# Kernel tuning notes

Measured on AMD Instinct MI355X. Metric: run time of the kernel, lower is better.

The kernel has to match this reference:

```python
import jax, jax.numpy as jnp
import numpy as np

TOP_K = 2
NUM_EXPERTS = 64
SEQ, BS, HS = 2048, 4, 4096
TOKENS = SEQ * BS  # tokens_per_batch
TOL = 1e-4
EPS = 1e-8


def sinkhorn(temp_cost):
    # temp_cost: (T, E) float32 logits. Mirrors SinkhornRouter.sinkhorn exactly.
    cost = jnp.exp(temp_cost)
    n0, n1 = cost.shape
    # initial d0 (overwritten inside loop in torch too, kept for fidelity of carry dtype/shape)
    d0 = (TOKENS / NUM_EXPERTS) * jnp.sum(jnp.exp(2.0 * temp_cost), axis=1)
    d1 = jnp.ones((n1,), dtype=cost.dtype)
    err0 = jnp.asarray(1e9, dtype=cost.dtype)

    def cond(carry):
        _, _, err = carry
        return err > TOL

    def body(carry):
        d0, d1, _ = carry  # d1 here plays the role of d1_old
        d0_new = (1.0 / n0) / (jnp.sum(d1 * cost, axis=1) + EPS)          # (T,)
        d1_new = (1.0 / n1) / (jnp.sum(d0_new[:, None] * cost, axis=0) + EPS)  # (E,)
        err = jnp.mean(jnp.abs(d1 - d1_new))
        return (d0_new, d1_new, err)

    d0, d1, _ = jax.lax.while_loop(cond, body, (d0, d1, err0))
    return d1 * cost * d0[:, None]


def setup_inputs() -> dict:
    key = jax.random.key(0)
    kx, kw = jax.random.split(key)
    x = jax.random.normal(kx, (SEQ, BS, HS), dtype=jnp.float32)
    W = jax.random.normal(kw, (NUM_EXPERTS, HS), dtype=jnp.float32) * 0.02
    return {"x": x, "W": W}


def reference(x, W):
    # router logits: (T, E)
    logits = jnp.reshape(x, (-1, x.shape[-1])) @ W.T
    # Sinkhorn normalization is done in fp32 under no_grad in torch -> stop_gradient
    norm_logits = sinkhorn(jax.lax.stop_gradient(logits).astype(jnp.float32))
    _, indices = jax.lax.top_k(norm_logits, TOP_K)  # (T, top_k) int32
    # top_k > 1 -> softmax activation (fp32, cast back)
    probs = jax.nn.softmax(logits.astype(jnp.float32), axis=-1).astype(logits.dtype)
    scores = jnp.take_along_axis(probs, indices, axis=1)  # (T, top_k)
    return scores, indices
```

## Files before the change

### kernel.cpp

```cpp
#include <hip/hip_runtime.h>
#include <hip/hip_cooperative_groups.h>
#include <math.h>

namespace cg = cooperative_groups;

namespace {
constexpr int kTokens = 8192;
constexpr int kHS = 4096;
constexpr float kTol = 1e-4f;
constexpr float kEps = 1e-8f;
constexpr int kMaxIters = 1000;
constexpr int kSinkBlocks = 32;
constexpr int kSplit = 4;
constexpr size_t kTagFloats = 128;
constexpr size_t kGdataFloats = 2 * 32 * 64;
constexpr size_t kPartOff = kTagFloats + kGdataFloats;
constexpr size_t kPartFloats = (size_t)kTokens * kSplit * 64;
constexpr size_t kWhiOff = kPartOff + kPartFloats;
constexpr size_t kWFragFloats = (size_t)(kHS / 32) * 4 * 64 * 4;
constexpr size_t kWloOff = kWhiOff + kWFragFloats;
constexpr size_t kWsNeedFloats = kWloOff + kWFragFloats;
constexpr size_t kWtpFloats = (size_t)(kHS / 4) * 64 * 4;
}

__device__ __forceinline__ float wave_sum(float v) {
#pragma unroll
  for (int o = 32; o; o >>= 1) v += __shfl_xor(v, o, 64);
  return v;
}

typedef __attribute__((ext_vector_type(8))) short bf16x8;
typedef __attribute__((ext_vector_type(4))) float f32x4;

__device__ __forceinline__ unsigned short f2bf(float x) {
  unsigned u = __builtin_bit_cast(unsigned, x);
  u += 0x7fffu + ((u >> 16) & 1u);
  return (unsigned short)(u >> 16);
}

__device__ __forceinline__ void split8r(const float4 a, const float4 b,
                                        bf16x8& hi, bf16x8& lo) {
  const float v[8] = {a.x, a.y, a.z, a.w, b.x, b.y, b.z, b.w};
#pragma unroll
  for (int j = 0; j < 8; ++j) {
    const unsigned short h = f2bf(v[j]);
    const float hf = __builtin_bit_cast(float, (unsigned)h << 16);
    hi[j] = (short)h;
    lo[j] = (short)f2bf(v[j] - hf);
  }
}

__device__ __forceinline__ void split8(const float* p, bf16x8& hi, bf16x8& lo) {
  split8r(*(const float4*)p, *(const float4*)(p + 4), hi, lo);
}

__global__ void __launch_bounds__(256)
k_wsplit(const float* __restrict__ W, bf16x8* __restrict__ whi,
         bf16x8* __restrict__ wlo) {
  const int idx = blockIdx.x * 256 + threadIdx.x;
  const int lane = idx & 63;
  const int n = (idx >> 6) & 3;
  const int kk = idx >> 8;
  const int e = 16 * n + (lane & 15);
  const int k = kk * 32 + ((lane >> 4) << 3);
  bf16x8 hi, lo;
  split8(W + (size_t)e * kHS + k, hi, lo);
  whi[idx] = hi;
  wlo[idx] = lo;
}

__device__ __forceinline__ void ldB(const bf16x8* __restrict__ bhp,
                                    const bf16x8* __restrict__ blp, int ks,
                                    bf16x8 (&bh)[4], bf16x8 (&bl)[4]) {
#pragma unroll
  for (int n = 0; n < 4; ++n) {
    bh[n] = bhp[(ks * 4 + n) * 64];
    bl[n] = blp[(ks * 4 + n) * 64];
  }
}

__device__ __forceinline__ void ldX(const float* __restrict__ xp, int ks,
                                    float4 (&x)[2][2]) {
#pragma unroll
  for (int m = 0; m < 2; ++m) {
    x[m][0] = *(const float4*)(xp + (size_t)(16 * m) * kHS + ks * 32);
    x[m][1] = *(const float4*)(xp + (size_t)(16 * m) * kHS + ks * 32 + 4);
  }
}

__device__ __forceinline__ void mstep(const float4 (&x)[2][2],
                                      const bf16x8 (&bh)[4],
                                      const bf16x8 (&bl)[4],
                                      f32x4 (&acc)[2][4]) {
#pragma unroll
  for (int m = 0; m < 2; ++m) {
    bf16x8 ah, al;
    split8r(x[m][0], x[m][1], ah, al);
#pragma unroll
    for (int n = 0; n < 4; ++n) {
      acc[m][n] =
          __builtin_amdgcn_mfma_f32_16x16x32_bf16(ah, bh[n], acc[m][n], 0, 0, 0);
      acc[m][n] =
          __builtin_amdgcn_mfma_f32_16x16x32_bf16(al, bh[n], acc[m][n], 0, 0, 0);
      acc[m][n] =
          __builtin_amdgcn_mfma_f32_16x16x32_bf16(ah, bl[n], acc[m][n], 0, 0, 0);
    }
  }
}

__global__ void __launch_bounds__(256, 3)
k_logits(const float* __restrict__ X, const bf16x8* __restrict__ whi,
         const bf16x8* __restrict__ wlo, float* __restrict__ part) {
  const int tid = threadIdx.x;
  const int lane = tid & 63;
  const int wid = tid >> 6;
  const int tile = blockIdx.x >> 2;
  const int sig = blockIdx.x & 3;
  const int t0 = tile * 32;
  const int r = lane & 15;
  const int g = lane >> 4;
  const int kk0 = sig * 32 + wid * 8;

  const float* xp = X + (size_t)(t0 + r) * kHS + kk0 * 32 + g * 8;
  const bf16x8* bhp = whi + (size_t)kk0 * 4 * 64 + lane;
  const bf16x8* blp = wlo + (size_t)kk0 * 4 * 64 + lane;

  f32x4 acc[2][4];
#pragma unroll
  for (int m = 0; m < 2; ++m)
#pragma unroll
    for (int n = 0; n < 4; ++n) acc[m][n] = (f32x4){0.f, 0.f, 0.f, 0.f};

  bf16x8 bhA[4], blA[4], bhB[4], blB[4];
  float4 xA[2][2], xB[2][2];
  ldB(bhp, blp, 0, bhA, blA);
  ldX(xp, 0, xA);

#pragma unroll
  for (int kp = 0; kp < 4; ++kp) {
    const int ks = 2 * kp;
    ldB(bhp, blp, ks + 1, bhB, blB);
    ldX(xp, ks + 1, xB);
    mstep(xA, bhA, blA, acc);
    if (ks + 2 < 8) {
      ldB(bhp, blp, ks + 2, bhA, blA);
      ldX(xp, ks + 2, xA);
    }
    mstep(xB, bhB, blB, acc);
  }

  __shared__ __align__(16) float red[4][32][68];
#pragma unroll
  for (int m = 0; m < 2; ++m)
#pragma unroll
    for (int n = 0; n < 4; ++n)
#pragma unroll
      for (int q = 0; q < 4; ++q)
        red[wid][m * 16 + g * 4 + q][n * 16 + r] = acc[m][n][q];
  __syncthreads();

#pragma unroll
  for (int rep = 0; rep < 2; ++rep) {
    const int idx = rep * 256 + tid;
    const int t = idx >> 4;
    const int e4 = (idx & 15) * 4;
    float4 s = *(const float4*)&red[0][t][e4];
#pragma unroll
    for (int w = 1; w < 4; ++w) {
      const float4 p = *(const float4*)&red[w][t][e4];
      s.x += p.x; s.y += p.y; s.z += p.z; s.w += p.w;
    }
    *(float4*)(part + ((size_t)(tile * 4 + sig) * 32 + t) * 64 + e4) = s;
  }
}

__global__ void __launch_bounds__(1024, 1)
k_sinkhorn(const float* __restrict__ part, float* __restrict__ out,
           unsigned* __restrict__ tags, float* __restrict__ gdata) {
  const int tid = threadIdx.x;
  const int lane = tid & 63;
  const int wid = __builtin_amdgcn_readfirstlane(tid >> 6);
  const int blk = blockIdx.x;
  __shared__ float lds[1024];

  const int t0 = blk * 256 + wid * 16;
  float lg[16], cst[16];
#pragma unroll
  for (int t = 0; t < 16; ++t) {
    const int row = t0 + t;
    const float* pb =
        part + ((size_t)(row >> 5) * (kSplit * 32) + (row & 31)) * 64 + lane;
    const float a = pb[0] + pb[2048] + pb[4096] + pb[6144];
    lg[t] = a;
    cst[t] = expf(a);
  }

  float d1 = 1.0f;
  float d0v[16];
  for (int it = 0; it < kMaxIters; ++it) {
    float p = 0.0f;
#pragma unroll
    for (int t = 0; t < 16; ++t) {
      const float s = wave_sum(d1 * cst[t]);
      const float d0t = (1.0f / 8192.0f) / (s + kEps);
      d0v[t] = d0t;
      p = fmaf(d0t, cst[t], p);
    }
    __syncthreads();
    lds[wid * 64 + lane] = p;
    __syncthreads();
    const unsigned want = (unsigned)(it + 1);
    const int buf = it & 1;
    if (wid == 0) {
      float bp = 0.0f;
#pragma unroll
      for (int w = 0; w < 16; ++w) bp += lds[w * 64 + lane];
      __hip_atomic_store(&gdata[((size_t)buf * 32 + blk) * 64 + lane], bp,
                         __ATOMIC_RELAXED, __HIP_MEMORY_SCOPE_AGENT);
      __threadfence();
      if (lane == 0)
        __hip_atomic_store(&tags[buf * 32 + blk], want, __ATOMIC_RELEASE,
                           __HIP_MEMORY_SCOPE_AGENT);
      if (lane < 32) {
        while (__hip_atomic_load(&tags[buf * 32 + lane], __ATOMIC_ACQUIRE,
                                 __HIP_MEMORY_SCOPE_AGENT) != want) {
          __builtin_amdgcn_s_sleep(1);
        }
      }
    }
    __syncthreads();
    float s2 = 0.0f;
#pragma unroll
    for (int i = 0; i < 2; ++i)
      s2 += __hip_atomic_load(
          &gdata[((size_t)buf * 32 + wid * 2 + i) * 64 + lane],
          __ATOMIC_RELAXED, __HIP_MEMORY_SCOPE_AGENT);
    lds[wid * 64 + lane] = s2;
    __syncthreads();
    float colsum = 0.0f;
#pragma unroll
    for (int w = 0; w < 16; ++w) colsum += lds[w * 64 + lane];
    const float d1n = (1.0f / 64.0f) / (colsum + kEps);
    const float err = wave_sum(fabsf(d1 - d1n)) * (1.0f / 64.0f);
    d1 = d1n;
    if (err <= kTol) break;
  }

#pragma unroll
  for (int t = 0; t < 16; ++t) {
    const float lgv = lg[t];
    float m = lgv;
#pragma unroll
    for (int o = 32; o; o >>= 1) m = fmaxf(m, __shfl_xor(m, o, 64));
    const float ex = expf(lgv - m);
    const float den = wave_sum(ex);
    const float prob = ex / den;

    const float v = (d1 * cst[t]) * d0v[t];
    float v1 = v;
    int i1 = lane;
#pragma unroll
    for (int o = 32; o; o >>= 1) {
      const float ov = __shfl_xor(v1, o, 64);
      const int oi = __shfl_xor(i1, o, 64);
      if (ov > v1 || (ov == v1 && oi < i1)) { v1 = ov; i1 = oi; }
    }
    float v2 = (lane == i1) ? -INFINITY : v;
    int i2 = lane;
#pragma unroll
    for (int o = 32; o; o >>= 1) {
      const float ov = __shfl_xor(v2, o, 64);
      const int oi = __shfl_xor(i2, o, 64);
      if (ov > v2 || (ov == v2 && oi < i2)) { v2 = ov; i2 = oi; }
    }
    const float p1 = __shfl(prob, i1, 64);
    const float p2 = __shfl(prob, i2, 64);
    if (lane == 0) {
      const int row = t0 + t;
      out[row * 2 + 0] = p1;
      out[row * 2 + 1] = p2;
      out[2 * kTokens + row * 2 + 0] = (float)i1;
      out[2 * kTokens + row * 2 + 1] = (float)i2;
    }
  }
}

__global__ void __launch_bounds__(256, 1)
sinkhorn_router(const float* __restrict__ X, const float* __restrict__ W,
                float* __restrict__ out, float* __restrict__ ws) {
  cg::grid_group grid = cg::this_grid();
  const int tid = threadIdx.x;
  const int lane = tid & 63;
  const int wid = __builtin_amdgcn_readfirstlane(tid >> 6);
  const int blk = blockIdx.x;

  float4* wtp = reinterpret_cast<float4*>(ws);
  float* gpart = ws + kWtpFloats;
  __shared__ float lds[256];

  {
    const int j = blk * 256 + tid;
    const int e = j & 63;
    const int k4 = j >> 6;
    wtp[j] = *reinterpret_cast<const float4*>(W + (size_t)e * kHS + 4 * (size_t)k4);
  }
  grid.sync();

  const int t0 = blk * 32 + wid * 8;
  const float* xb = X + (size_t)t0 * kHS;
  float lg[8];
#pragma unroll
  for (int t = 0; t < 8; ++t) lg[t] = 0.0f;

#pragma unroll 2
  for (int k4 = 0; k4 < kHS / 4; ++k4) {
    const float4 w = wtp[k4 * 64 + lane];
#pragma unroll
    for (int t = 0; t < 8; ++t) {
      const float* xr = xb + (size_t)t * kHS + 4 * (size_t)k4;
      float a = lg[t];
      a = fmaf(xr[0], w.x, a);
      a = fmaf(xr[1], w.y, a);
      a = fmaf(xr[2], w.z, a);
      a = fmaf(xr[3], w.w, a);
      lg[t] = a;
    }
  }

  float cst[8];
#pragma unroll
  for (int t = 0; t < 8; ++t) cst[t] = expf(lg[t]);

  float d1 = 1.0f;
  float d0v[8];
  int buf = 0;
  for (int it = 0; it < kMaxIters; ++it) {
    float p = 0.0f;
#pragma unroll
    for (int t = 0; t < 8; ++t) {
      const float s = wave_sum(d1 * cst[t]);
      const float d0t = (1.0f / 8192.0f) / (s + kEps);
      d0v[t] = d0t;
      p = fmaf(d0t, cst[t], p);
    }
    __syncthreads();
    lds[wid * 64 + lane] = p;
    __syncthreads();
    if (wid == 0) {
      const float bp =
          lds[lane] + lds[64 + lane] + lds[128 + lane] + lds[192 + lane];
      gpart[buf * (256 * 64) + blk * 64 + lane] = bp;
    }
    grid.sync();
    const float* gp = gpart + buf * (256 * 64);
    float s = 0.0f;
#pragma unroll 8
    for (int b = 0; b < 64; ++b) s += gp[(wid * 64 + b) * 64 + lane];
    lds[wid * 64 + lane] = s;
    __syncthreads();
    const float colsum =
        lds[lane] + lds[64 + lane] + lds[128 + lane] + lds[192 + lane];
    const float d1n = (1.0f / 64.0f) / (colsum + kEps);
    const float err = wave_sum(fabsf(d1 - d1n)) * (1.0f / 64.0f);
    d1 = d1n;
    buf ^= 1;
    if (err <= kTol) break;
  }

#pragma unroll
  for (int t = 0; t < 8; ++t) {
    const float lgv = lg[t];
    float m = lgv;
#pragma unroll
    for (int o = 32; o; o >>= 1) m = fmaxf(m, __shfl_xor(m, o, 64));
    const float ex = expf(lgv - m);
    const float den = wave_sum(ex);
    const float prob = ex / den;

    const float v = (d1 * cst[t]) * d0v[t];
    float v1 = v;
    int i1 = lane;
#pragma unroll
    for (int o = 32; o; o >>= 1) {
      const float ov = __shfl_xor(v1, o, 64);
      const int oi = __shfl_xor(i1, o, 64);
      if (ov > v1 || (ov == v1 && oi < i1)) { v1 = ov; i1 = oi; }
    }
    float v2 = (lane == i1) ? -INFINITY : v;
    int i2 = lane;
#pragma unroll
    for (int o = 32; o; o >>= 1) {
      const float ov = __shfl_xor(v2, o, 64);
      const int oi = __shfl_xor(i2, o, 64);
      if (ov > v2 || (ov == v2 && oi < i2)) { v2 = ov; i2 = oi; }
    }
    const float p1 = __shfl(prob, i1, 64);
    const float p2 = __shfl(prob, i2, 64);
    if (lane == 0) {
      const int row = t0 + t;
      out[row * 2 + 0] = p1;
      out[row * 2 + 1] = p2;
      out[2 * kTokens + row * 2 + 0] = (float)i1;
      out[2 * kTokens + row * 2 + 1] = (float)i2;
    }
  }
}

extern "C" void kernel_launch(void* const* d_in, const int* in_sizes, int n_in,
                              void* d_out, int out_size, void* d_ws,
                              size_t ws_size, hipStream_t stream) {
  const float* X = (const float*)d_in[0];
  const float* W = (const float*)d_in[1];
  float* out = (float*)d_out;
  float* ws = (float*)d_ws;

  const size_t need = kWsNeedFloats * sizeof(float);
  if (ws_size < need) {
    void* args[] = {(void*)&X, (void*)&W, (void*)&out, (void*)&ws};
    hipLaunchCooperativeKernel((const void*)sinkhorn_router, dim3(256),
                               dim3(256), args, 0, stream);
    return;
  }

  unsigned* tags = reinterpret_cast<unsigned*>(ws);
  float* gdata = ws + kTagFloats;
  float* part = ws + kPartOff;
  bf16x8* whi = reinterpret_cast<bf16x8*>(ws + kWhiOff);
  bf16x8* wlo = reinterpret_cast<bf16x8*>(ws + kWloOff);

  hipMemsetAsync(tags, 0, kTagFloats * sizeof(float), stream);
  hipLaunchKernelGGL(k_wsplit, dim3((kHS / 32) * 4 * 64 / 256), dim3(256), 0,
                     stream, W, whi, wlo);
  hipLaunchKernelGGL(k_logits, dim3((kTokens / 32) * kSplit), dim3(256), 0,
                     stream, X, whi, wlo, part);
  hipLaunchKernelGGL(k_sinkhorn, dim3(kSinkBlocks), dim3(1024), 0, stream,
                     part, out, tags, gdata);
}
```

Before: 261.0 us.

## Stage X and W tiles through double-buffered LDS in logits GEMM

```diff
diff --git a/kernel.cpp b/kernel.cpp
--- a/kernel.cpp
+++ b/kernel.cpp
@@ -69,109 +69,89 @@
   wlo[idx] = lo;
 }
 
-__device__ __forceinline__ void ldB(const bf16x8* __restrict__ bhp,
-                                    const bf16x8* __restrict__ blp, int ks,
-                                    bf16x8 (&bh)[4], bf16x8 (&bl)[4]) {
-#pragma unroll
-  for (int n = 0; n < 4; ++n) {
-    bh[n] = bhp[(ks * 4 + n) * 64];
-    bl[n] = blp[(ks * 4 + n) * 64];
-  }
-}
-
-__device__ __forceinline__ void ldX(const float* __restrict__ xp, int ks,
-                                    float4 (&x)[2][2]) {
-#pragma unroll
-  for (int m = 0; m < 2; ++m) {
-    x[m][0] = *(const float4*)(xp + (size_t)(16 * m) * kHS + ks * 32);
-    x[m][1] = *(const float4*)(xp + (size_t)(16 * m) * kHS + ks * 32 + 4);
-  }
-}
-
-__device__ __forceinline__ void mstep(const float4 (&x)[2][2],
-                                      const bf16x8 (&bh)[4],
-                                      const bf16x8 (&bl)[4],
-                                      f32x4 (&acc)[2][4]) {
-#pragma unroll
-  for (int m = 0; m < 2; ++m) {
-    bf16x8 ah, al;
-    split8r(x[m][0], x[m][1], ah, al);
-#pragma unroll
-    for (int n = 0; n < 4; ++n) {
-      acc[m][n] =
-          __builtin_amdgcn_mfma_f32_16x16x32_bf16(ah, bh[n], acc[m][n], 0, 0, 0);
-      acc[m][n] =
-          __builtin_amdgcn_mfma_f32_16x16x32_bf16(al, bh[n], acc[m][n], 0, 0, 0);
-      acc[m][n] =
-          __builtin_amdgcn_mfma_f32_16x16x32_bf16(ah, bl[n], acc[m][n], 0, 0, 0);
-    }
-  }
-}
-
 __global__ void __launch_bounds__(256, 3)
 k_logits(const float* __restrict__ X, const bf16x8* __restrict__ whi,
          const bf16x8* __restrict__ wlo, float* __restrict__ part) {
+  constexpr int kXS = 36;
+  constexpr int kBOffH = 64 * kXS;
+  constexpr int kBOffL = kBOffH + 1024;
+  constexpr int kBufF = kBOffL + 1024;
+  __shared__ __align__(16) float sm[2][kBufF];
+
   const int tid = threadIdx.x;
   const int lane = tid & 63;
   const int wid = tid >> 6;
   const int tile = blockIdx.x >> 2;
   const int sig = blockIdx.x & 3;
-  const int t0 = tile * 32;
-  const int r = lane & 15;
+  const int t0 = tile * 64;
+  const int r15 = lane & 15;
   const int g = lane >> 4;
-  const int kk0 = sig * 32 + wid * 8;
-
-  const float* xp = X + (size_t)(t0 + r) * kHS + kk0 * 32 + g * 8;
-  const bf16x8* bhp = whi + (size_t)kk0 * 4 * 64 + lane;
-  const bf16x8* blp = wlo + (size_t)kk0 * 4 * 64 + lane;
-
-  f32x4 acc[2][4];
-#pragma unroll
-  for (int m = 0; m < 2; ++m)
-#pragma unroll
-    for (int n = 0; n < 4; ++n) acc[m][n] = (f32x4){0.f, 0.f, 0.f, 0.f};
-
-  bf16x8 bhA[4], blA[4], bhB[4], blB[4];
-  float4 xA[2][2], xB[2][2];
-  ldB(bhp, blp, 0, bhA, blA);
-  ldX(xp, 0, xA);
-
-#pragma unroll
-  for (int kp = 0; kp < 4; ++kp) {
-    const int ks = 2 * kp;
-    ldB(bhp, blp, ks + 1, bhB, blB);
-    ldX(xp, ks + 1, xB);
-    mstep(xA, bhA, blA, acc);
-    if (ks + 2 < 8) {
-      ldB(bhp, blp, ks + 2, bhA, blA);
-      ldX(xp, ks + 2, xA);
-    }
-    mstep(xB, bhB, blB, acc);
-  }
-
-  __shared__ __align__(16) float red[4][32][68];
-#pragma unroll
-  for (int m = 0; m < 2; ++m)
-#pragma unroll
-    for (int n = 0; n < 4; ++n)
-#pragma unroll
-      for (int q = 0; q < 4; ++q)
-        red[wid][m * 16 + g * 4 + q][n * 16 + r] = acc[m][n][q];
+
+  const int srow = tid >> 3;
+  const int scol = (tid & 7) * 4;
+  const float* xsrc0 = X + (size_t)(t0 + srow) * kHS + sig * 1024 + scol;
+  const float* xsrc1 = xsrc0 + (size_t)32 * kHS;
+  const bf16x8* bhsrc = whi + (size_t)sig * 32 * 256 + tid;
+  const bf16x8* blsrc = wlo + (size_t)sig * 32 * 256 + tid;
+
+  f32x4 acc[4];
+#pragma unroll
+  for (int n = 0; n < 4; ++n) acc[n] = (f32x4){0.f, 0.f, 0.f, 0.f};
+
+  {
+    const float4 xv0 = *(const float4*)xsrc0;
+    const float4 xv1 = *(const float4*)xsrc1;
+    const bf16x8 bhv = bhsrc[0];
+    const bf16x8 blv = blsrc[0];
+    *(float4*)&sm[0][srow * kXS + scol] = xv0;
+    *(float4*)&sm[0][(srow + 32) * kXS + scol] = xv1;
+    *(bf16x8*)&sm[0][kBOffH + tid * 4] = bhv;
+    *(bf16x8*)&sm[0][kBOffL + tid * 4] = blv;
+  }
   __syncthreads();
 
-#pragma unroll
-  for (int rep = 0; rep < 2; ++rep) {
-    const int idx = rep * 256 + tid;
-    const int t = idx >> 4;
-    const int e4 = (idx & 15) * 4;
-    float4 s = *(const float4*)&red[0][t][e4];
-#pragma unroll
-    for (int w = 1; w < 4; ++w) {
-      const float4 p = *(const float4*)&red[w][t][e4];
-      s.x += p.x; s.y += p.y; s.z += p.z; s.w += p.w;
-    }
-    *(float4*)(part + ((size_t)(tile * 4 + sig) * 32 + t) * 64 + e4) = s;
-  }
+  const int aoff = (16 * wid + r15) * kXS + g * 8;
+
+#pragma unroll 2
+  for (int ks = 0; ks < 32; ++ks) {
+    const int cur = ks & 1;
+    const bool more = (ks + 1) < 32;
+    float4 xv0, xv1;
+    bf16x8 bhv, blv;
+    if (more) {
+      xv0 = *(const float4*)(xsrc0 + (ks + 1) * 32);
+      xv1 = *(const float4*)(xsrc1 + (ks + 1) * 32);
+      bhv = bhsrc[(ks + 1) * 256];
+      blv = blsrc[(ks + 1) * 256];
+    }
+    const float4 a0 = *(const float4*)&sm[cur][aoff];
+    const float4 a1 = *(const float4*)&sm[cur][aoff + 4];
+    bf16x8 ah, al;
+    split8r(a0, a1, ah, al);
+#pragma unroll
+    for (int n = 0; n < 4; ++n) {
+      const bf16x8 bh = *(const bf16x8*)&sm[cur][kBOffH + (n * 64 + lane) * 4];
+      const bf16x8 bl = *(const bf16x8*)&sm[cur][kBOffL + (n * 64 + lane) * 4];
+      acc[n] = __builtin_amdgcn_mfma_f32_16x16x32_bf16(ah, bh, acc[n], 0, 0, 0);
+      acc[n] = __builtin_amdgcn_mfma_f32_16x16x32_bf16(al, bh, acc[n], 0, 0, 0);
+      acc[n] = __builtin_amdgcn_mfma_f32_16x16x32_bf16(ah, bl, acc[n], 0, 0, 0);
+    }
+    if (more) {
+      const int nb = cur ^ 1;
+      *(float4*)&sm[nb][srow * kXS + scol] = xv0;
+      *(float4*)&sm[nb][(srow + 32) * kXS + scol] = xv1;
+      *(bf16x8*)&sm[nb][kBOffH + tid * 4] = bhv;
+      *(bf16x8*)&sm[nb][kBOffL + tid * 4] = blv;
+    }
+    __syncthreads();
+  }
+
+  float* pb = part + ((size_t)(tile * 4 + sig) * 64 + 16 * wid) * 64;
+#pragma unroll
+  for (int n = 0; n < 4; ++n)
+#pragma unroll
+    for (int q = 0; q < 4; ++q)
+      pb[(size_t)(4 * g + q) * 64 + 16 * n + r15] = acc[n][q];
 }
 
 __global__ void __launch_bounds__(1024, 1)
@@ -189,8 +169,8 @@
   for (int t = 0; t < 16; ++t) {
     const int row = t0 + t;
     const float* pb =
-        part + ((size_t)(row >> 5) * (kSplit * 32) + (row & 31)) * 64 + lane;
-    const float a = pb[0] + pb[2048] + pb[4096] + pb[6144];
+        part + ((size_t)(row >> 6) * 256 + (row & 63)) * 64 + lane;
+    const float a = pb[0] + pb[4096] + pb[8192] + pb[12288];
     lg[t] = a;
     cst[t] = expf(a);
   }
@@ -431,7 +411,7 @@
   hipMemsetAsync(tags, 0, kTagFloats * sizeof(float), stream);
   hipLaunchKernelGGL(k_wsplit, dim3((kHS / 32) * 4 * 64 / 256), dim3(256), 0,
                      stream, W, whi, wlo);
-  hipLaunchKernelGGL(k_logits, dim3((kTokens / 32) * kSplit), dim3(256), 0,
+  hipLaunchKernelGGL(k_logits, dim3((kTokens / 64) * kSplit), dim3(256), 0,
                      stream, X, whi, wlo, part);
   hipLaunchKernelGGL(k_sinkhorn, dim3(kSinkBlocks), dim3(1024), 0, stream,
                      part, out, tags, gdata);
```

New measurement: 261.4 us. Within noise of the previous version (+0.2%).
